# Performance work log

Measured on AMD Instinct MI355X. Metric: run time of the kernel, lower is better.

Reference implementation:

```python
import jax, jax.numpy as jnp
import numpy as np

B, S, D, H = 2, 2048, 1024, 16
DK = D // H


def setup_inputs() -> dict:
    key = jax.random.key(0)
    ks = jax.random.split(key, 9)
    def xavier(k, shape):
        fan_in, fan_out = shape[1], shape[0]
        lim = jnp.sqrt(6.0 / (fan_in + fan_out))
        return jax.random.uniform(k, shape, jnp.float32, -lim, lim)
    x = jax.random.normal(ks[0], (B, S, D), jnp.float32)
    mask = jnp.ones((B, 1, S), jnp.int32)
    Wq = xavier(ks[1], (D, D)); bq = jnp.zeros((D,), jnp.float32)
    Wk = xavier(ks[2], (D, D)); bk = jnp.zeros((D,), jnp.float32)
    Wv = xavier(ks[3], (D, D)); bv = jnp.zeros((D,), jnp.float32)
    Wo = xavier(ks[4], (D, D)); bo = jnp.zeros((D,), jnp.float32)
    return {"x": x, "mask": mask, "Wq": Wq, "bq": bq, "Wk": Wk, "bk": bk,
            "Wv": Wv, "bv": bv, "Wo": Wo, "bo": bo}


def reference(x, mask, Wq, bq, Wk, bk, Wv, bv, Wo, bo):
    # Linear layers use torch convention y = x @ W.T + b
    q = (x @ Wq.T + bq).reshape(B, S, H, DK).transpose(0, 2, 1, 3)  # [B,H,S,DK]
    k = (x @ Wk.T + bk).reshape(B, S, H, DK).transpose(0, 2, 1, 3)
    v = (x @ Wv.T + bv).reshape(B, S, H, DK).transpose(0, 2, 1, 3)
    scores = jnp.einsum('bhqd,bhkd->bhqk', q, k) / jnp.sqrt(jnp.float32(DK))
    m = mask[:, None, :, :]  # unsqueeze(1): broadcast over heads -> [B,1,1,S]
    scores = jnp.where(m == 0, jnp.float32(-1e9), scores)
    p = jax.nn.softmax(scores, axis=-1)  # dropout p=0.0 -> identity
    ctx = jnp.einsum('bhqk,bhkd->bhqd', p, v)
    ctx = ctx.transpose(0, 2, 1, 3).reshape(B, S, D)
    return ctx @ Wo.T + bo
```

## Files before the change

kernel.cpp:

```cpp
#include <hip/hip_runtime.h>
#include <hip/hip_bf16.h>
#include <math.h>

#define Bn 2
#define Sn 2048
#define Dn 1024
#define Hn 16
#define DKn 64

using fragb  = __attribute__((ext_vector_type(8))) short;
using frag16 = __attribute__((ext_vector_type(8))) _Float16;
using f4     = __attribute__((ext_vector_type(4))) float;

__device__ __forceinline__ short f2bf(float f) {
    union { float f; unsigned u; } v; v.f = f;
    unsigned r = v.u + 0x7FFF + ((v.u >> 16) & 1);
    return (short)(r >> 16);
}
__device__ __forceinline__ short f2h(float f) {
    _Float16 h = (_Float16)f;
    short s; __builtin_memcpy(&s, &h, 2); return s;
}

#define GLOAD(gptr, lptr)                                                     \
    __builtin_amdgcn_global_load_lds(                                         \
        (const __attribute__((address_space(1))) unsigned int*)(const void*)(gptr), \
        (__attribute__((address_space(3))) unsigned int*)(void*)(lptr), 16, 0, 0)

#define NX (Bn * Sn * Dn)
#define NW (Dn * Dn)

__global__ __launch_bounds__(256) void prep(
    const float* __restrict__ x,  const float* __restrict__ Wq,
    const float* __restrict__ Wk, const float* __restrict__ Wv,
    const float* __restrict__ Wo, const int* __restrict__ mask,
    short* __restrict__ xh,
    short* __restrict__ Wqh, short* __restrict__ Wkh,
    short* __restrict__ Wvh, short* __restrict__ Woh,
    short* __restrict__ mfb)
{
    int i = blockIdx.x * 256 + threadIdx.x;
    const float* src; short* dst; int j;
    if (i < NX)               { src = x;  dst = xh;  j = i; }
    else if (i < NX + NW)     { src = Wq; dst = Wqh; j = i - NX; }
    else if (i < NX + 2 * NW) { src = Wk; dst = Wkh; j = i - NX - NW; }
    else if (i < NX + 3 * NW) { src = Wv; dst = Wvh; j = i - NX - 2 * NW; }
    else if (i < NX + 4 * NW) { src = Wo; dst = Woh; j = i - NX - 3 * NW; }
    else {
        j = i - NX - 4 * NW;
        if (j < Bn * Sn) mfb[j] = mask[j] ? (short)0x3F80 : (short)0;
        return;
    }
    dst[j] = f2h(src[j]);
}

#define BN 128
#define BK 64

template <int BMT>
__global__ __launch_bounds__(256) void gemm_mfma(
    const short* __restrict__ A,
    const short* __restrict__ W0, const float* __restrict__ b0,
    const short* __restrict__ W1, const float* __restrict__ b1,
    const short* __restrict__ W2, const float* __restrict__ b2,
    const int* __restrict__ mask,
    short* __restrict__ Qb, short* __restrict__ Kb, short* __restrict__ Vtb,
    float* __restrict__ outf, int mode)
{
    constexpr int MI = BMT / 32;
    __shared__ __align__(16) short As[BMT * BK];
    __shared__ __align__(16) short Bs[BN * BK];

    const int tid  = threadIdx.x;
    const int wave = tid >> 6;
    const int lane = tid & 63;
    const int quad = lane >> 4;
    const int l16  = lane & 15;
    const int wm   = wave >> 1;
    const int wn   = wave & 1;

    const int m0   = blockIdx.y * BMT;
    const int n0   = blockIdx.x * BN;
    const int widx = n0 >> 10;
    const int nl0  = n0 & 1023;

    const short* Wp   = widx == 0 ? W0 : (widx == 1 ? W1 : W2);
    const float* bias = widx == 0 ? b0 : (widx == 1 ? b1 : b2);

    f4 acc[MI][4];
    #pragma unroll
    for (int i = 0; i < MI; i++)
        #pragma unroll
        for (int j = 0; j < 4; j++) {
            acc[i][j][0] = 0.f; acc[i][j][1] = 0.f;
            acc[i][j][2] = 0.f; acc[i][j][3] = 0.f;
        }

    const int K = Dn;
    const int lr = lane >> 3;
    const int sc = ((lane & 7) ^ lr) * 8;
    const short* Apl = A  + (size_t)(m0  + lr) * K + sc;
    const short* Bpl = Wp + (size_t)(nl0 + lr) * K + sc;

    const int ca0 = ((quad ^ (l16 & 7)) * 8);
    const int ca1 = (((quad + 4) ^ (l16 & 7)) * 8);

    for (int k0 = 0; k0 < K; k0 += BK) {
        __syncthreads();
        if constexpr (BMT == 128) {
            #pragma unroll
            for (int g = 0; g < 4; g++)
                GLOAD(Apl + (size_t)(wave * 32 + g * 8) * K + k0,
                      &As[(wave * 32 + g * 8) * BK]);
        } else {
            #pragma unroll
            for (int g = 0; g < 2; g++)
                GLOAD(Apl + (size_t)(wave * 16 + g * 8) * K + k0,
                      &As[(wave * 16 + g * 8) * BK]);
        }
        #pragma unroll
        for (int g = 0; g < 4; g++)
            GLOAD(Bpl + (size_t)(wave * 32 + g * 8) * K + k0,
                  &Bs[(wave * 32 + g * 8) * BK]);
        __syncthreads();

        #pragma unroll
        for (int ki = 0; ki < 2; ki++) {
            const int ca = ki ? ca1 : ca0;
            frag16 a[MI], b[4];
            #pragma unroll
            for (int mi = 0; mi < MI; mi++)
                a[mi] = *(const frag16*)&As[(wm * (BMT / 2) + mi * 16 + l16) * BK + ca];
            #pragma unroll
            for (int ni = 0; ni < 4; ni++)
                b[ni] = *(const frag16*)&Bs[(wn * 64 + ni * 16 + l16) * BK + ca];
            #pragma unroll
            for (int mi = 0; mi < MI; mi++)
                #pragma unroll
                for (int ni = 0; ni < 4; ni++)
                    acc[mi][ni] = __builtin_amdgcn_mfma_f32_16x16x32_f16(
                        a[mi], b[ni], acc[mi][ni], 0, 0, 0);
        }
    }

    const float QSCALE = 0.125f * 1.44269504088896340736f;

    #pragma unroll
    for (int mi = 0; mi < MI; mi++) {
        #pragma unroll
        for (int ni = 0; ni < 4; ni++) {
            int nl = nl0 + wn * 64 + ni * 16 + l16;
            float bv = bias[nl];
            #pragma unroll
            for (int r = 0; r < 4; r++) {
                int m = m0 + wm * (BMT / 2) + mi * 16 + quad * 4 + r;
                float v = acc[mi][ni][r] + bv;
                if (mode == 0) {
                    int b  = m >> 11, s = m & (Sn - 1);
                    int h  = nl >> 6, dk = nl & 63;
                    if (widx == 0)
                        Qb[((size_t)(b * Hn + h) * Sn + s) * DKn + dk] = f2bf(v * QSCALE);
                    else if (widx == 1)
                        Kb[((size_t)(b * Hn + h) * Sn + s) * DKn + dk] = f2bf(v);
                    else {
                        float mv = (float)mask[b * Sn + s];
                        Vtb[((size_t)(b * Hn + h) * DKn + dk) * Sn + s] = f2bf(v * mv);
                    }
                } else {
                    outf[(size_t)m * Dn + nl] = v;
                }
            }
        }
    }
}

#define LP  72

__global__ __launch_bounds__(256) void attn_mfma(
    const short* __restrict__ Qb, const short* __restrict__ Kb,
    const short* __restrict__ Vtb, const short* __restrict__ mfb,
    short* __restrict__ ctxh)
{
    __shared__ __align__(16) short Ks[64 * 64];
    __shared__ __align__(16) short Vs[64 * 64];
    __shared__ short Ps[4][32 * LP];
    __shared__ __align__(16) short mfs[64];

    const int tid  = threadIdx.x;
    const int wave = tid >> 6;
    const int lane = tid & 63;
    const int quad = lane >> 4;
    const int l16  = lane & 15;

    const int qt  = blockIdx.x & 15;
    const int bhh = blockIdx.x >> 4;
    const int b   = bhh >> 4;
    const int h   = bhh & 15;

    fragb qf[2][2];
    #pragma unroll
    for (int w = 0; w < 2; w++) {
        int qrow = qt * 128 + wave * 32 + w * 16 + l16;
        const short* qptr = Qb + ((size_t)bhh * Sn + qrow) * DKn + quad * 8;
        qf[w][0] = *(const fragb*)(qptr);
        qf[w][1] = *(const fragb*)(qptr + 32);
    }

    f4 ctx[2][4];
    #pragma unroll
    for (int w = 0; w < 2; w++)
        #pragma unroll
        for (int dt = 0; dt < 4; dt++) {
            ctx[w][dt][0] = 0.f; ctx[w][dt][1] = 0.f;
            ctx[w][dt][2] = 0.f; ctx[w][dt][3] = 0.f;
        }
    f4 lacc[2];
    lacc[0][0] = 0.f; lacc[0][1] = 0.f; lacc[0][2] = 0.f; lacc[0][3] = 0.f;
    lacc[1] = lacc[0];

    const int lr = lane >> 3;
    const int sc = ((lane & 7) ^ lr) * 8;
    const short* Kg = Kb  + (size_t)bhh * Sn * DKn;
    const short* Vg = Vtb + (size_t)bhh * DKn * Sn;
    const short* mg = mfb + (size_t)b * Sn;

    const short* Ksrc = Kg + (size_t)(wave * 16 + lr) * DKn + sc;
    const short* Vsrc = Vg + (size_t)(wave * 16 + lr) * Sn + sc;

    const int c0 = ((quad ^ (l16 & 7)) * 8);

    for (int kt = 0; kt < Sn / 64; kt++) {
        __syncthreads();
        GLOAD(Ksrc + (size_t)kt * 4096,             &Ks[(wave * 16) * 64]);
        GLOAD(Ksrc + (size_t)kt * 4096 + 8 * DKn,   &Ks[(wave * 16 + 8) * 64]);
        GLOAD(Vsrc + (size_t)kt * 64,               &Vs[(wave * 16) * 64]);
        GLOAD(Vsrc + (size_t)kt * 64 + 8 * Sn,      &Vs[(wave * 16 + 8) * 64]);
        if (tid < 8)
            *(uint4*)&mfs[tid * 8] = *(const uint4*)(mg + kt * 64 + tid * 8);
        __syncthreads();

        #pragma unroll
        for (int t = 0; t < 4; t++) {
            fragb k0 = *(const fragb*)&Ks[(t * 16 + l16) * 64 + c0];
            fragb k1 = *(const fragb*)&Ks[(t * 16 + l16) * 64 + (c0 ^ 32)];
            #pragma unroll
            for (int w = 0; w < 2; w++) {
                f4 a; a[0] = 0.f; a[1] = 0.f; a[2] = 0.f; a[3] = 0.f;
                a = __builtin_amdgcn_mfma_f32_16x16x32_bf16(k0, qf[w][0], a, 0, 0, 0);
                a = __builtin_amdgcn_mfma_f32_16x16x32_bf16(k1, qf[w][1], a, 0, 0, 0);
                unsigned u0 = __float_as_uint(exp2f(a[0]));
                unsigned u1 = __float_as_uint(exp2f(a[1]));
                unsigned u2 = __float_as_uint(exp2f(a[2]));
                unsigned u3 = __float_as_uint(exp2f(a[3]));
                uint2 pw;
                pw.x = __builtin_amdgcn_perm(u1, u0, 0x07060302u);
                pw.y = __builtin_amdgcn_perm(u3, u2, 0x07060302u);
                *(uint2*)&Ps[wave][(w * 16 + l16) * LP + 16 * t + quad * 4] = pw;
            }
        }

        fragb p[2][2];
        #pragma unroll
        for (int w = 0; w < 2; w++) {
            p[w][0] = *(const fragb*)&Ps[wave][(w * 16 + l16) * LP + quad * 8];
            p[w][1] = *(const fragb*)&Ps[wave][(w * 16 + l16) * LP + quad * 8 + 32];
        }
        fragb m0 = *(const fragb*)&mfs[quad * 8];
        fragb m1 = *(const fragb*)&mfs[quad * 8 + 32];
        #pragma unroll
        for (int w = 0; w < 2; w++) {
            lacc[w] = __builtin_amdgcn_mfma_f32_16x16x32_bf16(p[w][0], m0, lacc[w], 0, 0, 0);
            lacc[w] = __builtin_amdgcn_mfma_f32_16x16x32_bf16(p[w][1], m1, lacc[w], 0, 0, 0);
        }
        #pragma unroll
        for (int dt = 0; dt < 4; dt++) {
            fragb v0 = *(const fragb*)&Vs[(dt * 16 + l16) * 64 + c0];
            fragb v1 = *(const fragb*)&Vs[(dt * 16 + l16) * 64 + (c0 ^ 32)];
            #pragma unroll
            for (int w = 0; w < 2; w++) {
                ctx[w][dt] = __builtin_amdgcn_mfma_f32_16x16x32_bf16(p[w][0], v0, ctx[w][dt], 0, 0, 0);
                ctx[w][dt] = __builtin_amdgcn_mfma_f32_16x16x32_bf16(p[w][1], v1, ctx[w][dt], 0, 0, 0);
            }
        }
    }

    #pragma unroll
    for (int w = 0; w < 2; w++)
        #pragma unroll
        for (int r = 0; r < 4; r++) {
            float inv = 1.f / lacc[w][r];
            int row = qt * 128 + wave * 32 + w * 16 + quad * 4 + r;
            #pragma unroll
            for (int dt = 0; dt < 4; dt++) {
                float val = ctx[w][dt][r] * inv;
                size_t idx = ((size_t)(b * Sn + row)) * Dn + h * DKn + dt * 16 + l16;
                ctxh[idx] = f2h(val);
            }
        }
}

extern "C" void kernel_launch(void* const* d_in, const int* in_sizes, int n_in,
                              void* d_out, int out_size, void* d_ws, size_t ws_size,
                              hipStream_t stream) {
    const float* x    = (const float*)d_in[0];
    const int*   mask = (const int*)d_in[1];
    const float* Wq   = (const float*)d_in[2];
    const float* bq   = (const float*)d_in[3];
    const float* Wk   = (const float*)d_in[4];
    const float* bk   = (const float*)d_in[5];
    const float* Wv   = (const float*)d_in[6];
    const float* bv   = (const float*)d_in[7];
    const float* Wo   = (const float*)d_in[8];
    const float* bo   = (const float*)d_in[9];
    float* out = (float*)d_out;

    char* ws = (char*)d_ws;
    const size_t MB = 1024u * 1024u;
    short* xh  = (short*)(ws + 0 * MB);
    short* Wqh = (short*)(ws + 8 * MB);
    short* Wkh = (short*)(ws + 10 * MB);
    short* Wvh = (short*)(ws + 12 * MB);
    short* Woh = (short*)(ws + 14 * MB);
    short* Qb  = (short*)(ws + 16 * MB);
    short* Kb  = (short*)(ws + 24 * MB);
    short* Vtb = (short*)(ws + 32 * MB);
    short* Ch  = (short*)(ws + 40 * MB);
    short* mfb = (short*)(ws + 48 * MB);

    const int TOT = NX + 4 * NW + Bn * Sn;
    prep<<<(TOT + 255) / 256, 256, 0, stream>>>(
        x, Wq, Wk, Wv, Wo, mask, xh, Wqh, Wkh, Wvh, Woh, mfb);

    gemm_mfma<128><<<dim3(24, 32), 256, 0, stream>>>(
        xh, Wqh, bq, Wkh, bk, Wvh, bv, mask,
        Qb, Kb, Vtb, nullptr, 0);

    attn_mfma<<<dim3(Bn * Hn * (Sn / 128)), 256, 0, stream>>>(
        Qb, Kb, Vtb, mfb, Ch);

    gemm_mfma<64><<<dim3(8, 64), 256, 0, stream>>>(
        Ch, Woh, bo, Woh, bo, Woh, bo, mask,
        nullptr, nullptr, nullptr, out, 1);
}
```

Measured before the change: 228.1 us.

## Split attention over two key halves and reduce partial contexts

The attention kernel now splits each query tile's key range into two halves handled by separate blocks, doubling the grid from 512 to 1024 blocks. Each block writes unnormalized fp32 context and row sums, and a new reduce kernel sums the halves, normalizes and converts to half. This targets low occupancy across the GPU's compute units, at the cost of extra fp32 global traffic (two 16MB partial buffers), an extra launch and workspace reshuffling. The softmax has no max subtraction, so partial sums combine directly.

```diff
diff --git a/kernel.cpp b/kernel.cpp
--- a/kernel.cpp
+++ b/kernel.cpp
@@ -7,6 +7,7 @@
 #define Dn 1024
 #define Hn 16
 #define DKn 64
+#define BHS (Bn * Hn * Sn)
 
 using fragb  = __attribute__((ext_vector_type(8))) short;
 using frag16 = __attribute__((ext_vector_type(8))) _Float16;
@@ -179,7 +180,8 @@
 __global__ __launch_bounds__(256) void attn_mfma(
     const short* __restrict__ Qb, const short* __restrict__ Kb,
     const short* __restrict__ Vtb, const short* __restrict__ mfb,
-    short* __restrict__ ctxh)
+    float* __restrict__ ctxp0, float* __restrict__ ctxp1,
+    float* __restrict__ lp)
 {
     __shared__ __align__(16) short Ks[64 * 64];
     __shared__ __align__(16) short Vs[64 * 64];
@@ -192,8 +194,10 @@
     const int quad = lane >> 4;
     const int l16  = lane & 15;
 
-    const int qt  = blockIdx.x & 15;
-    const int bhh = blockIdx.x >> 4;
+    const int split = blockIdx.x & 1;
+    const int rest  = blockIdx.x >> 1;
+    const int qt  = rest & 15;
+    const int bhh = rest >> 4;
     const int b   = bhh >> 4;
     const int h   = bhh & 15;
 
@@ -229,7 +233,8 @@
 
     const int c0 = ((quad ^ (l16 & 7)) * 8);
 
-    for (int kt = 0; kt < Sn / 64; kt++) {
+    const int kt0 = split * 16;
+    for (int kt = kt0; kt < kt0 + 16; kt++) {
         __syncthreads();
         GLOAD(Ksrc + (size_t)kt * 4096,             &Ks[(wave * 16) * 64]);
         GLOAD(Ksrc + (size_t)kt * 4096 + 8 * DKn,   &Ks[(wave * 16 + 8) * 64]);
@@ -284,19 +289,43 @@
         }
     }
 
+    float* cp  = split ? ctxp1 : ctxp0;
+    float* lpp = lp + (size_t)split * BHS;
     #pragma unroll
     for (int w = 0; w < 2; w++)
         #pragma unroll
         for (int r = 0; r < 4; r++) {
-            float inv = 1.f / lacc[w][r];
             int row = qt * 128 + wave * 32 + w * 16 + quad * 4 + r;
-            #pragma unroll
-            for (int dt = 0; dt < 4; dt++) {
-                float val = ctx[w][dt][r] * inv;
-                size_t idx = ((size_t)(b * Sn + row)) * Dn + h * DKn + dt * 16 + l16;
-                ctxh[idx] = f2h(val);
-            }
-        }
+            if (l16 == 0) lpp[(size_t)bhh * Sn + row] = lacc[w][r];
+            #pragma unroll
+            for (int dt = 0; dt < 4; dt++)
+                cp[((size_t)(b * Sn + row)) * Dn + h * DKn + dt * 16 + l16] =
+                    ctx[w][dt][r];
+        }
+}
+
+__global__ __launch_bounds__(256) void reduce_ctx(
+    const float* __restrict__ c0, const float* __restrict__ c1,
+    const float* __restrict__ lp, short* __restrict__ Ch)
+{
+    int i4 = blockIdx.x * 256 + threadIdx.x;
+    int e    = i4 << 2;
+    int brow = e >> 10;
+    int d    = e & 1023;
+    int b    = brow >> 11;
+    int row  = brow & (Sn - 1);
+    int h    = d >> 6;
+    size_t li = (size_t)(b * Hn + h) * Sn + row;
+    float l = lp[li] + lp[BHS + li];
+    float inv = 1.f / l;
+    float4 v0 = ((const float4*)c0)[i4];
+    float4 v1 = ((const float4*)c1)[i4];
+    ushort4 o;
+    o.x = (unsigned short)f2h((v0.x + v1.x) * inv);
+    o.y = (unsigned short)f2h((v0.y + v1.y) * inv);
+    o.z = (unsigned short)f2h((v0.z + v1.z) * inv);
+    o.w = (unsigned short)f2h((v0.w + v1.w) * inv);
+    ((ushort4*)Ch)[i4] = o;
 }
 
 extern "C" void kernel_launch(void* const* d_in, const int* in_sizes, int n_in,
@@ -316,16 +345,19 @@
 
     char* ws = (char*)d_ws;
     const size_t MB = 1024u * 1024u;
-    short* xh  = (short*)(ws + 0 * MB);
-    short* Wqh = (short*)(ws + 8 * MB);
-    short* Wkh = (short*)(ws + 10 * MB);
-    short* Wvh = (short*)(ws + 12 * MB);
-    short* Woh = (short*)(ws + 14 * MB);
-    short* Qb  = (short*)(ws + 16 * MB);
-    short* Kb  = (short*)(ws + 24 * MB);
-    short* Vtb = (short*)(ws + 32 * MB);
-    short* Ch  = (short*)(ws + 40 * MB);
-    short* mfb = (short*)(ws + 48 * MB);
+    short* xh    = (short*)(ws + 0 * MB);
+    short* Wqh   = (short*)(ws + 8 * MB);
+    short* Wkh   = (short*)(ws + 10 * MB);
+    short* Wvh   = (short*)(ws + 12 * MB);
+    short* Qb    = (short*)(ws + 16 * MB);
+    short* Kb    = (short*)(ws + 24 * MB);
+    short* Vtb   = (short*)(ws + 32 * MB);
+    float* ctxp0 = (float*)(ws + 0 * MB);
+    float* ctxp1 = (float*)(ws + 40 * MB);
+    short* Woh   = (short*)(ws + 56 * MB);
+    float* lp    = (float*)(ws + 58 * MB);
+    short* mfb   = (short*)(ws + 59 * MB);
+    short* Ch    = (short*)(ws + 60 * MB);
 
     const int TOT = NX + 4 * NW + Bn * Sn;
     prep<<<(TOT + 255) / 256, 256, 0, stream>>>(
@@ -335,8 +367,10 @@
         xh, Wqh, bq, Wkh, bk, Wvh, bv, mask,
         Qb, Kb, Vtb, nullptr, 0);
 
-    attn_mfma<<<dim3(Bn * Hn * (Sn / 128)), 256, 0, stream>>>(
-        Qb, Kb, Vtb, mfb, Ch);
+    attn_mfma<<<dim3(Bn * Hn * (Sn / 128) * 2), 256, 0, stream>>>(
+        Qb, Kb, Vtb, mfb, ctxp0, ctxp1, lp);
+
+    reduce_ctx<<<dim3(NX / 4 / 256), 256, 0, stream>>>(ctxp0, ctxp1, lp, Ch);
 
     gemm_mfma<64><<<dim3(8, 64), 256, 0, stream>>>(
         Ch, Woh, bo, Woh, bo, Woh, bo, mask,
```

Result: no change. 225.6 us (-1.1%).
